# Kernel tuning notes

Hardware: AMD Instinct MI355X
Metric: run time of the kernel (lower is better)

## Reference

```python
import jax, jax.numpy as jnp
import numpy as np

K = 256
NUM_SAMPLES = 256
SIGMA = 0.05
B, D = 64, 2048


def setup_inputs() -> dict:
    key = jax.random.key(0)
    k1, k2 = jax.random.split(key)
    x = jax.random.normal(k1, (B, D), dtype=jnp.float32)
    noise = jax.random.normal(k2, (B, NUM_SAMPLES, D), dtype=jnp.float32)
    return {"x": x, "noise": noise}


def reference(x, noise):
    b, d = x.shape
    ns = noise.shape[1]
    # perturbed scores: (b, ns, d)
    perturbed = x[:, None, :] + noise * SIGMA
    # top-k indices per sample (order irrelevant for counting)
    _, idx = jax.lax.top_k(perturbed, K)  # (b, ns, K)
    # Count how often each position is in the top-k, averaged over samples.
    # Equivalent to mean over ns of one_hot(sorted_indices).sum(axis=k-dim),
    # without materializing the (b, ns, K, d) one-hot tensor.
    bi = jnp.arange(b)[:, None, None]  # (b,1,1) broadcast over (ns, K)
    counts = jnp.zeros((b, d), dtype=jnp.float32).at[bi, idx].add(1.0)
    topk_indicators = counts / jnp.asarray(ns, jnp.float32)  # (b, d)
    # Non-top-k one-hot mean: each sample contributes 1 at every non-selected
    # position, so the mean over samples is exactly 1 - topk mean.
    non_topk_indicators = 1.0 - topk_indicators
    return (topk_indicators, non_topk_indicators)
```

## Files before the change

### kernel.cpp

```cpp
#include <hip/hip_runtime.h>

#define DD    2048
#define KK    256
#define NS    256
#define BB    64
#define WPB   4
#define SPB   WPB
#define NG    (NS / SPB)
#define ROWS  NG
#define RBYTES (DD / 2)
#define NBIN  256
#define WHALF 0.5f
#define FSCALE 256.0f
#define CWAVE 32
#define PSEGW 17

__device__ __forceinline__ uint32_t orderable(float f) {
    uint32_t u = __float_as_uint(f);
    return (u & 0x80000000u) ? ~u : (u | 0x80000000u);
}
__device__ __forceinline__ float inv_orderable(uint32_t u) {
    return (u & 0x80000000u) ? __uint_as_float(u & 0x7FFFFFFFu)
                             : __uint_as_float(~u);
}

__global__ __launch_bounds__(256) void thresh_kernel(
    const float* __restrict__ x, float* __restrict__ tEst)
{
    const int tid  = threadIdx.x;
    const int b    = blockIdx.x;
    const int lane = tid & 63;
    const int wid  = tid >> 6;
    __shared__ uint32_t hist[256 * PSEGW];
    __shared__ uint32_t wsum[4];

    #pragma unroll
    for (int i = 0; i < PSEGW; ++i) hist[tid * PSEGW + i] = 0u;
    __syncthreads();

    const float4* xr = (const float4*)(x + (size_t)b * DD);
    float4 a0 = xr[tid * 2 + 0], a1 = xr[tid * 2 + 1];
    uint32_t u[8];
    u[0] = orderable(a0.x); u[1] = orderable(a0.y);
    u[2] = orderable(a0.z); u[3] = orderable(a0.w);
    u[4] = orderable(a1.x); u[5] = orderable(a1.y);
    u[6] = orderable(a1.z); u[7] = orderable(a1.w);
    #pragma unroll
    for (int e = 0; e < 8; ++e) {
        uint32_t bkt = u[e] >> 20;
        atomicAdd(&hist[(bkt >> 4) * PSEGW + (bkt & 15u)], 1u);
    }
    __syncthreads();

    uint32_t h[16], seg = 0;
    #pragma unroll
    for (int i = 0; i < 16; ++i) { h[i] = hist[tid * PSEGW + i]; seg += h[i]; }
    uint32_t sfx = seg;
    #pragma unroll
    for (int st = 1; st < 64; st <<= 1) {
        uint32_t o = __shfl_down(sfx, (unsigned)st, 64);
        if (lane + st < 64) sfx += o;
    }
    if (lane == 0) wsum[wid] = sfx;
    __syncthreads();
    uint32_t hi = 0;
    #pragma unroll
    for (int w = 0; w < 4; ++w) if (w > wid) hi += wsum[w];
    const uint32_t incl  = sfx + hi;
    const uint32_t above = incl - seg;
    if (above < KK && incl >= KK) {
        uint32_t c = above;
        #pragma unroll
        for (int i = 15; i >= 0; --i) {
            if (c + h[i] >= KK) {
                tEst[b] = inv_orderable(((uint32_t)(tid * 16 + i)) << 20);
                break;
            }
            c += h[i];
        }
    }
}

#define BIN1(Q, COMP)                                                   \
    { float val = v[Q].COMP;                                            \
      if (val >= lo) {                                                  \
          int r = (int)((val - lo) * FSCALE);                           \
          if (r >= NBIN) ++W; else atomicAdd(&myHist[r], 1u);           \
      } }
#define BIN4(Q) BIN1(Q, x) BIN1(Q, y) BIN1(Q, z) BIN1(Q, w)

#define CLS1(Q, J, COMP)                                                \
    { float val = v[Q].COMP;                                            \
      if (val >= lo) {                                                  \
          int r = (int)((val - lo) * FSCALE);                           \
          int d = ((Q) << 8) + lane * 4 + (J);                          \
          if (r > tb) {                                                 \
              atomicAdd(&counts[d], 1u);                                \
          } else if (r == tb) {                                         \
              uint32_t jj = atomicAdd(myCandCnt, 1u);                   \
              if (jj < CWAVE) { myCf[jj] = val; myCd[jj] = (uint32_t)d; } \
          }                                                             \
      } }
#define CLS4(Q) CLS1(Q, 0, x) CLS1(Q, 1, y) CLS1(Q, 2, z) CLS1(Q, 3, w)

template <int USE_WS>
__global__ __launch_bounds__(256) void topk_wave_kernel(
    const float* __restrict__ x,
    const float* __restrict__ noise,
    const float* __restrict__ tEst,
    unsigned char* __restrict__ ws,
    float* __restrict__ outCounts)
{
    const int tid  = threadIdx.x;
    const int bg   = blockIdx.x;
    const int b    = bg >> 6;
    const int g    = bg & (NG - 1);
    const int lane = tid & 63;
    const int wid  = tid >> 6;

    __shared__ uint32_t counts[DD];
    __shared__ uint32_t hist[WPB * NBIN];
    __shared__ float    cand_f[WPB * CWAVE];
    __shared__ uint32_t cand_d[WPB * CWAVE];
    __shared__ uint32_t candCnt[WPB];

    uint32_t* myHist    = hist + wid * NBIN;
    float*    myCf      = cand_f + wid * CWAVE;
    uint32_t* myCd      = cand_d + wid * CWAVE;
    uint32_t* myCandCnt = &candCnt[wid];

    const uint4 z = make_uint4(0u, 0u, 0u, 0u);
    uint4* c4 = (uint4*)counts;
    c4[tid] = z; c4[tid + 256] = z;
    ((uint4*)hist)[tid] = z;
    if (tid < WPB) candCnt[tid] = 0u;

    const float lo = tEst[b] - WHALF;

    const float4* xr = (const float4*)(x + (size_t)b * DD);
    float4 xv[8];
    #pragma unroll
    for (int q = 0; q < 8; ++q) xv[q] = xr[q * 64 + lane];

    const float4* nr =
        (const float4*)(noise + ((size_t)b * NS + (size_t)g * SPB + wid) * DD);

    __syncthreads();

    float4 v[8];
    #pragma unroll
    for (int q = 0; q < 8; ++q) v[q] = nr[q * 64 + lane];
    #pragma unroll
    for (int q = 0; q < 8; ++q) {
        v[q].x = fmaf(v[q].x, 0.05f, xv[q].x);
        v[q].y = fmaf(v[q].y, 0.05f, xv[q].y);
        v[q].z = fmaf(v[q].z, 0.05f, xv[q].z);
        v[q].w = fmaf(v[q].w, 0.05f, xv[q].w);
    }

    uint32_t W = 0;
    BIN4(0) BIN4(1) BIN4(2) BIN4(3) BIN4(4) BIN4(5) BIN4(6) BIN4(7)
    #pragma unroll
    for (int st = 32; st >= 1; st >>= 1)
        W += __shfl_down(W, (unsigned)st, 64);
    W = __shfl(W, 0, 64);

    uint4 hh = *(const uint4*)&myHist[lane * 4];
    const uint32_t h0 = hh.x, h1 = hh.y, h2 = hh.z, h3 = hh.w;
    uint32_t seg = h0 + h1 + h2 + h3;
    uint32_t sfx = seg;
    #pragma unroll
    for (int st = 1; st < 64; st <<= 1) {
        uint32_t o = __shfl_down(sfx, (unsigned)st, 64);
        if (lane + st < 64) sfx += o;
    }
    const uint32_t incl  = sfx + W;
    const uint32_t above = incl - seg;

    bool cross = (above < KK && incl >= KK);
    unsigned long long mask = __ballot(cross);
    int tbl = NBIN + 1; uint32_t Rl = 0;
    if (cross) {
        uint32_t c = above;
        if (c + h3 >= KK)                { tbl = lane * 4 + 3; Rl = KK - c; }
        else if (c + h3 + h2 >= KK)      { tbl = lane * 4 + 2; Rl = KK - c - h3; }
        else if (c + h3 + h2 + h1 >= KK) { tbl = lane * 4 + 1; Rl = KK - c - h3 - h2; }
        else                             { tbl = lane * 4 + 0; Rl = KK - c - h3 - h2 - h1; }
    }
    int srcl = mask ? (__ffsll((long long)mask) - 1) : 0;
    int      tb = __shfl(tbl, srcl, 64);
    uint32_t R  = __shfl(Rl,  srcl, 64);
    if (!mask) { tb = NBIN + 1; R = 0; }

    CLS4(0) CLS4(1) CLS4(2) CLS4(3) CLS4(4) CLS4(5) CLS4(6) CLS4(7)

    uint32_t M = *myCandCnt;
    if (M > CWAVE) M = CWAVE;
    if ((uint32_t)lane < M) {
        float    vv = myCf[lane];
        uint32_t dj = myCd[lane];
        uint32_t r  = 0;
        for (uint32_t i = 0; i < M; ++i) {
            float vi = myCf[i];
            r += (vi > vv) || (vi == vv && myCd[i] < dj);
        }
        if (r < R) atomicAdd(&counts[dj], 1u);
    }
    __syncthreads();

    if (USE_WS) {
        uint32_t p = 0;
        #pragma unroll
        for (int n = 0; n < 8; ++n)
            p |= (counts[tid * 8 + n] & 0xFu) << (4 * n);
        ((uint32_t*)(ws + ((size_t)b * ROWS + g) * RBYTES))[tid] = p;
    } else {
        float* rowOut = outCounts + (size_t)b * DD;
        #pragma unroll
        for (int e = 0; e < 8; ++e) {
            uint32_t c = counts[tid * 8 + e];
            if (c) atomicAdd(&rowOut[tid * 8 + e], (float)c);
        }
    }
}

__global__ __launch_bounds__(256) void reduce_kernel(
    const unsigned char* __restrict__ ws, float* __restrict__ out)
{
    int idx = blockIdx.x * 256 + threadIdx.x;
    int b   = idx >> 8;
    int t8  = idx & 255;
    const uint32_t* base =
        (const uint32_t*)(ws + (size_t)b * ROWS * RBYTES) + t8;

    uint32_t s0 = 0, s1 = 0, s2 = 0, s3 = 0, s4 = 0, s5 = 0, s6 = 0, s7 = 0;
    #pragma unroll
    for (int half = 0; half < 2; ++half) {
        uint32_t accLo = 0, accHi = 0;
        #pragma unroll 8
        for (int g = 0; g < ROWS / 2; ++g) {
            uint32_t p = base[(size_t)(half * (ROWS / 2) + g) * (RBYTES / 4)];
            accLo += p & 0x0F0F0F0Fu;
            accHi += (p >> 4) & 0x0F0F0F0Fu;
        }
        s0 += accLo & 0xFFu;         s1 += accHi & 0xFFu;
        s2 += (accLo >> 8) & 0xFFu;  s3 += (accHi >> 8) & 0xFFu;
        s4 += (accLo >> 16) & 0xFFu; s5 += (accHi >> 16) & 0xFFu;
        s6 += (accLo >> 24) & 0xFFu; s7 += (accHi >> 24) & 0xFFu;
    }

    const float inv = 1.0f / 256.0f;
    float4 ta = make_float4(s0 * inv, s1 * inv, s2 * inv, s3 * inv);
    float4 tb = make_float4(s4 * inv, s5 * inv, s6 * inv, s7 * inv);
    float* o0 = out + (size_t)b * DD + (size_t)t8 * 8;
    float* o1 = o0 + (size_t)(BB * DD);
    *(float4*)(o0)     = ta;
    *(float4*)(o0 + 4) = tb;
    *(float4*)(o1)     = make_float4(1.0f - ta.x, 1.0f - ta.y, 1.0f - ta.z, 1.0f - ta.w);
    *(float4*)(o1 + 4) = make_float4(1.0f - tb.x, 1.0f - tb.y, 1.0f - tb.z, 1.0f - tb.w);
}

__global__ __launch_bounds__(256) void finalize_kernel(float* __restrict__ out) {
    int i = blockIdx.x * 256 + threadIdx.x;
    float t = out[i] * (1.0f / 256.0f);
    out[i] = t;
    out[BB * DD + i] = 1.0f - t;
}

extern "C" void kernel_launch(void* const* d_in, const int* in_sizes, int n_in,
                              void* d_out, int out_size, void* d_ws, size_t ws_size,
                              hipStream_t stream) {
    const float* x     = (const float*)d_in[0];
    const float* noise = (const float*)d_in[1];
    float* out = (float*)d_out;

    const size_t partials = (size_t)BB * ROWS * RBYTES;
    if (ws_size >= partials + BB * sizeof(float)) {
        unsigned char* ws8 = (unsigned char*)d_ws;
        float* tEst = (float*)(ws8 + partials);
        thresh_kernel<<<BB, 256, 0, stream>>>(x, tEst);
        topk_wave_kernel<1><<<BB * NG, 256, 0, stream>>>(x, noise, tEst, ws8, nullptr);
        reduce_kernel<<<(BB * DD / 8) / 256, 256, 0, stream>>>(ws8, out);
    } else {
        float* tEst = (float*)d_ws;
        hipMemsetAsync(out, 0, (size_t)BB * DD * sizeof(float), stream);
        thresh_kernel<<<BB, 256, 0, stream>>>(x, tEst);
        topk_wave_kernel<0><<<BB * NG, 256, 0, stream>>>(x, noise, tEst, nullptr, out);
        finalize_kernel<<<(BB * DD) / 256, 256, 0, stream>>>(out);
    }
}
```

Baseline: 44.31 us.

## Replace shared count atomics with per-lane bitmasks and stage x through LDS

Each lane now marks its selected positions in a 32-bit register mask instead of issuing shared-memory atomicAdd into a 2048-entry counts array. Tie-break winners are folded into the owning lane's mask via a ballot loop, and the per-wave masks are combined through a small LDS table when packing 4-bit counts. The x row is staged cooperatively in shared memory rather than held in registers, noise loads are issued before the barrier, and launch bounds request higher occupancy. This targets LDS atomic traffic, the zeroing of the counts array, and register pressure, at the cost of extra bit manipulation and a serial ballot loop over winners.

```diff
diff --git a/kernel.cpp b/kernel.cpp
--- a/kernel.cpp
+++ b/kernel.cpp
@@ -93,18 +93,20 @@
     { float val = v[Q].COMP;                                            \
       if (val >= lo) {                                                  \
           int r = (int)((val - lo) * FSCALE);                           \
-          int d = ((Q) << 8) + lane * 4 + (J);                          \
           if (r > tb) {                                                 \
-              atomicAdd(&counts[d], 1u);                                \
+              cmask |= (1u << ((Q) * 4 + (J)));                         \
           } else if (r == tb) {                                         \
               uint32_t jj = atomicAdd(myCandCnt, 1u);                   \
-              if (jj < CWAVE) { myCf[jj] = val; myCd[jj] = (uint32_t)d; } \
+              if (jj < CWAVE) {                                         \
+                  myCf[jj] = val;                                       \
+                  myCd[jj] = (uint32_t)(((Q) << 8) + lane * 4 + (J));   \
+              }                                                         \
           }                                                             \
       } }
 #define CLS4(Q) CLS1(Q, 0, x) CLS1(Q, 1, y) CLS1(Q, 2, z) CLS1(Q, 3, w)
 
 template <int USE_WS>
-__global__ __launch_bounds__(256) void topk_wave_kernel(
+__global__ __launch_bounds__(256, 8) void topk_wave_kernel(
     const float* __restrict__ x,
     const float* __restrict__ noise,
     const float* __restrict__ tEst,
@@ -118,44 +120,43 @@
     const int lane = tid & 63;
     const int wid  = tid >> 6;
 
-    __shared__ uint32_t counts[DD];
+    __shared__ float    xs[DD];
     __shared__ uint32_t hist[WPB * NBIN];
     __shared__ float    cand_f[WPB * CWAVE];
     __shared__ uint32_t cand_d[WPB * CWAVE];
     __shared__ uint32_t candCnt[WPB];
+    __shared__ uint32_t wmaskLDS[WPB][64];
 
     uint32_t* myHist    = hist + wid * NBIN;
     float*    myCf      = cand_f + wid * CWAVE;
     uint32_t* myCd      = cand_d + wid * CWAVE;
     uint32_t* myCandCnt = &candCnt[wid];
 
-    const uint4 z = make_uint4(0u, 0u, 0u, 0u);
-    uint4* c4 = (uint4*)counts;
-    c4[tid] = z; c4[tid + 256] = z;
-    ((uint4*)hist)[tid] = z;
-    if (tid < WPB) candCnt[tid] = 0u;
-
-    const float lo = tEst[b] - WHALF;
-
-    const float4* xr = (const float4*)(x + (size_t)b * DD);
-    float4 xv[8];
-    #pragma unroll
-    for (int q = 0; q < 8; ++q) xv[q] = xr[q * 64 + lane];
-
     const float4* nr =
         (const float4*)(noise + ((size_t)b * NS + (size_t)g * SPB + wid) * DD);
-
-    __syncthreads();
-
     float4 v[8];
     #pragma unroll
     for (int q = 0; q < 8; ++q) v[q] = nr[q * 64 + lane];
+
+    const float4* xr = (const float4*)(x + (size_t)b * DD);
+    float4* xs4 = (float4*)xs;
+    xs4[tid]       = xr[tid];
+    xs4[tid + 256] = xr[tid + 256];
+
+    const uint4 z = make_uint4(0u, 0u, 0u, 0u);
+    *(uint4*)&myHist[lane * 4] = z;
+    if (lane == 0) *myCandCnt = 0u;
+
+    const float lo = tEst[b] - WHALF;
+    __syncthreads();
+
     #pragma unroll
     for (int q = 0; q < 8; ++q) {
-        v[q].x = fmaf(v[q].x, 0.05f, xv[q].x);
-        v[q].y = fmaf(v[q].y, 0.05f, xv[q].y);
-        v[q].z = fmaf(v[q].z, 0.05f, xv[q].z);
-        v[q].w = fmaf(v[q].w, 0.05f, xv[q].w);
+        float4 xq = xs4[q * 64 + lane];
+        v[q].x = fmaf(v[q].x, 0.05f, xq.x);
+        v[q].y = fmaf(v[q].y, 0.05f, xq.y);
+        v[q].z = fmaf(v[q].z, 0.05f, xq.z);
+        v[q].w = fmaf(v[q].w, 0.05f, xq.w);
     }
 
     uint32_t W = 0;
@@ -192,10 +193,12 @@
     uint32_t R  = __shfl(Rl,  srcl, 64);
     if (!mask) { tb = NBIN + 1; R = 0; }
 
+    uint32_t cmask = 0;
     CLS4(0) CLS4(1) CLS4(2) CLS4(3) CLS4(4) CLS4(5) CLS4(6) CLS4(7)
 
     uint32_t M = *myCandCnt;
     if (M > CWAVE) M = CWAVE;
+    uint32_t win = 0;
     if ((uint32_t)lane < M) {
         float    vv = myCf[lane];
         uint32_t dj = myCd[lane];
@@ -204,22 +207,45 @@
             float vi = myCf[i];
             r += (vi > vv) || (vi == vv && myCd[i] < dj);
         }
-        if (r < R) atomicAdd(&counts[dj], 1u);
-    }
+        win = (r < R);
+    }
+    unsigned long long wm = __ballot(win);
+    while (wm) {
+        int j = __ffsll((long long)wm) - 1;
+        wm &= wm - 1;
+        uint32_t dj = myCd[j];
+        if (lane == (int)((dj >> 2) & 63u))
+            cmask |= 1u << (((dj >> 8) << 2) | (dj & 3u));
+    }
+
+    wmaskLDS[wid][lane] = cmask;
     __syncthreads();
 
     if (USE_WS) {
+        const uint32_t base_e = (uint32_t)(tid >> 5) << 2;
+        const uint32_t l0 = (uint32_t)(tid * 2) & 63u;
+        const uint32_t l1 = (uint32_t)(tid * 2 + 1) & 63u;
         uint32_t p = 0;
         #pragma unroll
-        for (int n = 0; n < 8; ++n)
-            p |= (counts[tid * 8 + n] & 0xFu) << (4 * n);
+        for (int w = 0; w < WPB; ++w) {
+            uint32_t m0 = wmaskLDS[w][l0];
+            uint32_t m1 = wmaskLDS[w][l1];
+            p += ((m0 >> (base_e + 0)) & 1u) << 0;
+            p += ((m0 >> (base_e + 1)) & 1u) << 4;
+            p += ((m0 >> (base_e + 2)) & 1u) << 8;
+            p += ((m0 >> (base_e + 3)) & 1u) << 12;
+            p += ((m1 >> (base_e + 0)) & 1u) << 16;
+            p += ((m1 >> (base_e + 1)) & 1u) << 20;
+            p += ((m1 >> (base_e + 2)) & 1u) << 24;
+            p += ((m1 >> (base_e + 3)) & 1u) << 28;
+        }
         ((uint32_t*)(ws + ((size_t)b * ROWS + g) * RBYTES))[tid] = p;
     } else {
         float* rowOut = outCounts + (size_t)b * DD;
         #pragma unroll
-        for (int e = 0; e < 8; ++e) {
-            uint32_t c = counts[tid * 8 + e];
-            if (c) atomicAdd(&rowOut[tid * 8 + e], (float)c);
+        for (int e = 0; e < 32; ++e) {
+            if ((cmask >> e) & 1u)
+                atomicAdd(&rowOut[(e >> 2) * 256 + lane * 4 + (e & 3)], 1.0f);
         }
     }
 }
```

Result: slower. 62.18 us (+40.3%).
